# Kernel tuning notes

Hardware: AMD Instinct MI355X
Metric: run time of the kernel (lower is better)

## Reference

```python
import jax, jax.numpy as jnp
import numpy as np

HEAD_DIM = 128
INFTY_APPROX = 1e+30
ROTARY_BASE = 10000.0

B, T, M = 2, 2048, 1024
H = M // HEAD_DIM  # 8


def setup_inputs() -> dict:
    key = jax.random.key(0)
    ks = jax.random.split(key, 5)
    x = jax.random.normal(ks[0], (B, T, M), dtype=jnp.float32)
    # mu-param inits: wq zeros in the original; use small random here for a
    # non-degenerate numerical baseline, scaled like kv_init = d_model**-0.5
    scale = M ** (-0.5)
    wq = jax.random.normal(ks[1], (M, H, HEAD_DIM), dtype=jnp.float32) * scale
    wk = jax.random.normal(ks[2], (M, H, HEAD_DIM), dtype=jnp.float32) * scale
    wv = jax.random.normal(ks[3], (M, H, HEAD_DIM), dtype=jnp.float32) * scale
    wo = jax.random.normal(ks[4], (H, HEAD_DIM, M), dtype=jnp.float32) * scale
    return {"x": x, "wq": wq, "wk": wk, "wv": wv, "wo": wo}


def _rotary(x, base=ROTARY_BASE):
    # x: [..., T, W]; non-interpretable RoPE over even/odd halves of W
    length, width = x.shape[-2], x.shape[-1]
    half = width // 2
    positions = jnp.arange(length)[:, None].astype(x.dtype)          # [T,1]
    ang_freqs = jnp.power(base, -jnp.arange(half) / half)[None, :]   # [1,half]
    radians = positions * ang_freqs                                  # [T,half]
    cos = jnp.cos(radians).astype(x.dtype)
    sin = jnp.sin(radians).astype(x.dtype)
    even, odd = jnp.split(x, 2, axis=-1)
    return jnp.concatenate([even * cos - odd * sin,
                            even * sin + odd * cos], axis=-1)


def _fractional_rotary(x):
    # rotary on first half of head dim, passthrough on the rest
    rot, skip = jnp.split(x, 2, axis=-1)
    return jnp.concatenate([_rotary(rot), skip], axis=-1)


def reference(x, wq, wk, wv, wo):
    q = jnp.einsum('bim,mhd->bhid', x, wq)
    k = jnp.einsum('bim,mhd->bhid', x, wk)
    v = jnp.einsum('bim,mhd->bhid', x, wv)
    q = _fractional_rotary(q)
    k = _fractional_rotary(k)
    # mu-param attention: scale by 1/HEAD_DIM (not 1/sqrt(D))
    s = jnp.einsum('bhid,bhjd->bhij', q, k) / HEAD_DIM
    i = jnp.arange(T)[:, None]
    j = jnp.arange(T)[None, :]
    mask = (i < j).astype(s.dtype)  # strictly-upper-triangular
    s = s - jnp.asarray(INFTY_APPROX, dtype=s.dtype) * mask
    p = jax.nn.softmax(s, axis=-1)
    o = jnp.einsum('bhij,bhjd->bhid', p, v)
    r = jnp.einsum('bhid,hdm->bim', o, wo)
    return r
```

## Files before the change

kernel.cpp:

```cpp
#include <hip/hip_runtime.h>

#define T_SEQ 2048
#define MDL   1024
#define NH    8
#define HD    128
#define SPLIT 4

typedef __bf16 bf16;
typedef __bf16 bf16x8 __attribute__((ext_vector_type(8)));
typedef __bf16 bf16x4 __attribute__((ext_vector_type(4)));
typedef float  f32x4  __attribute__((ext_vector_type(4)));

#define GLB(p) ((const __attribute__((address_space(1))) void*)(p))
#define LDS(p) ((__attribute__((address_space(3))) void*)(p))

#if __has_builtin(__builtin_amdgcn_exp2f)
#define EXP2(x) __builtin_amdgcn_exp2f(x)
#else
#define EXP2(x) __expf((x) * 0.6931471805599453f)
#endif

#define QSCALE 0.011271055f


__global__ __launch_bounds__(256) void prep_kernel(
    const float* __restrict__ x,
    const float* __restrict__ wq, const float* __restrict__ wk,
    const float* __restrict__ wv, const float* __restrict__ wo,
    bf16* __restrict__ xb, bf16* __restrict__ Wt, bf16* __restrict__ Wot)
{
    __shared__ bf16 t_lds[64 * 72];
    const int tid = threadIdx.x;
    if (blockIdx.x < 2048) {
        size_t i = ((size_t)blockIdx.x * 256 + tid) * 8;
        float4 v0 = *(const float4*)(x + i);
        float4 v1 = *(const float4*)(x + i + 4);
        bf16x8 o;
        o[0]=(bf16)v0.x; o[1]=(bf16)v0.y; o[2]=(bf16)v0.z; o[3]=(bf16)v0.w;
        o[4]=(bf16)v1.x; o[5]=(bf16)v1.y; o[6]=(bf16)v1.z; o[7]=(bf16)v1.w;
        *(bf16x8*)(xb + i) = o;
        return;
    }
    const int bx = blockIdx.x - 2048;
    const int sec = bx >> 8;
    const int tile = bx & 255;
    const int k0 = (tile >> 4) * 64, n0 = (tile & 15) * 64;
    const float* src = sec == 0 ? wq : sec == 1 ? wk : sec == 2 ? wv : wo;
    bf16* dst = sec < 3 ? (Wt + (size_t)sec * MDL * MDL) : Wot;

    const int ir = tid >> 2, jc = (tid & 3) * 16;
    const float* sp = src + (size_t)(k0 + ir) * MDL + n0 + jc;
    #pragma unroll
    for (int c = 0; c < 4; ++c) {
        float4 v = *(const float4*)(sp + c * 4);
        bf16x4 o; o[0]=(bf16)v.x; o[1]=(bf16)v.y; o[2]=(bf16)v.z; o[3]=(bf16)v.w;
        *(bf16x4*)&t_lds[ir * 72 + jc + c * 4] = o;
    }
    __syncthreads();
    bf16x8 o0, o1;
    #pragma unroll
    for (int jj = 0; jj < 8; ++jj) {
        o0[jj] = t_lds[(jc + jj) * 72 + ir];
        o1[jj] = t_lds[(jc + 8 + jj) * 72 + ir];
    }
    bf16* dp = dst + (size_t)(n0 + ir) * MDL + k0 + jc;
    *(bf16x8*)dp = o0;
    *(bf16x8*)(dp + 8) = o1;
}

__global__ __launch_bounds__(256) void qkv_rope_kernel(
    const bf16* __restrict__ xb, const bf16* __restrict__ Wt,
    bf16* __restrict__ Qb, bf16* __restrict__ Kt, bf16* __restrict__ Vt)
{
    __shared__ bf16 smem[16384];
    bf16* a_lds = smem;
    bf16* b_lds = smem + 8192;

    const int tid = threadIdx.x, bx = blockIdx.x;
    const int nt = bx % 24, mt = bx / 24;
    const int n0 = nt * 128, m0 = mt * 128;
    const int section = n0 >> 10;
    const int h = (n0 & 1023) >> 7;

    const int lane = tid & 63, w = tid >> 6;
    const int quad = lane >> 4, l15 = lane & 15;
    const int wr = w >> 1, wc = w & 1;
    const int srow = lane >> 3;

    const int csw = ((lane & 7) ^ srow) * 8;
    const bf16* gA = xb + (size_t)m0 * MDL + csw;
    const bf16* gB = Wt + (size_t)n0 * MDL + csw;

    f32x4 acc[4][4] = {};

    for (int k0 = 0; k0 < MDL; k0 += 64) {
        #pragma unroll
        for (int i = 0; i < 4; ++i) {
            const int ch = w * 4 + i;
            const int row = ch * 8 + srow;
            __builtin_amdgcn_global_load_lds(GLB(gA + (size_t)row * MDL + k0),
                                             LDS(&a_lds[ch * 512]), 16, 0, 0);
            __builtin_amdgcn_global_load_lds(GLB(gB + (size_t)row * MDL + k0),
                                             LDS(&b_lds[ch * 512]), 16, 0, 0);
        }
        __syncthreads();

        #pragma unroll
        for (int hh = 0; hh < 2; ++hh) {
            bf16x8 af[4], bfr[4];
            #pragma unroll
            for (int mi = 0; mi < 4; ++mi) {
                const int ra = wr * 64 + mi * 16 + l15;
                af[mi] = *(const bf16x8*)&a_lds[ra * 64 + ((hh * 4 + quad) ^ (ra & 7)) * 8];
            }
            #pragma unroll
            for (int ni = 0; ni < 4; ++ni) {
                const int rb = wc * 64 + ni * 16 + l15;
                bfr[ni] = *(const bf16x8*)&b_lds[rb * 64 + ((hh * 4 + quad) ^ (rb & 7)) * 8];
            }
            #pragma unroll
            for (int mi = 0; mi < 4; ++mi)
                #pragma unroll
                for (int ni = 0; ni < 4; ++ni)
                    acc[mi][ni] = __builtin_amdgcn_mfma_f32_16x16x32_bf16(af[mi], bfr[ni], acc[mi][ni], 0, 0, 0);
        }
        __syncthreads();
    }

    const int bdx = m0 >> 11;
    const int t0 = m0 & (T_SEQ - 1);
    const int bh = bdx * NH + h;

    if (section == 2) {
        #pragma unroll
        for (int c = 0; c < 2; ++c) {
            if (wc == c) {
                #pragma unroll
                for (int mi = 0; mi < 4; ++mi)
                    #pragma unroll
                    for (int r = 0; r < 4; ++r) {
                        int p = 16 * quad + 4 * r + mi;
                        int base = (wr * 8 + (p >> 3)) * 512 + (p & 7);
                        #pragma unroll
                        for (int ni = 0; ni < 4; ++ni)
                            smem[base + (ni * 16 + l15) * 8] = (bf16)acc[mi][ni][r];
                    }
            }
            __syncthreads();
            {
                const int t8 = tid >> 4;
                bf16* vp = Vt + ((size_t)(bh * 32 + (t0 >> 6) + (t8 >> 3))) * 8192
                              + (t8 & 7) * 1024 + c * 512 + (tid & 15) * 32;
                #pragma unroll
                for (int k = 0; k < 4; ++k)
                    *(bf16x8*)(vp + k * 8) = *(const bf16x8*)&smem[tid * 32 + k * 8];
            }
            __syncthreads();
        }
        return;
    }

    float fr_n[2];
    #pragma unroll
    for (int ni = 0; ni < 2; ++ni)
        fr_n[ni] = __expf(-(float)(ni * 16 + l15) * 0.28782313662425573f);

    if (section == 0) {
        #pragma unroll
        for (int mi = 0; mi < 4; ++mi) {
            #pragma unroll
            for (int r = 0; r < 4; ++r) {
                int t = t0 + wr * 64 + mi * 16 + quad * 4 + r;
                bf16* orow = Qb + ((size_t)bh * T_SEQ + t) * HD;
                if (wc == 0) {
                    #pragma unroll
                    for (int ni = 0; ni < 2; ++ni) {
                        int d = ni * 16 + l15;
                        float ang = (float)t * fr_n[ni];
                        float sn = __sinf(ang), cs = __cosf(ang);
                        float ev = acc[mi][ni][r];
                        float ov = acc[mi][ni + 2][r];
                        orow[d]      = (bf16)((ev * cs - ov * sn) * QSCALE);
                        orow[d + 32] = (bf16)((ev * sn + ov * cs) * QSCALE);
                    }
                } else {
                    #pragma unroll
                    for (int ni = 0; ni < 4; ++ni)
                        orow[64 + ni * 16 + l15] = (bf16)(acc[mi][ni][r] * QSCALE);
                }
            }
        }
    } else {
        #pragma unroll
        for (int c = 0; c < 2; ++c) {
            if (wr == c) {
                #pragma unroll
                for (int mi = 0; mi < 4; ++mi) {
                    #pragma unroll
                    for (int r = 0; r < 4; ++r) {
                        int tl = mi * 16 + quad * 4 + r;
                        int t = t0 + c * 64 + tl;
                        if (wc == 0) {
                            #pragma unroll
                            for (int ni = 0; ni < 2; ++ni) {
                                int d = ni * 16 + l15;
                                float ang = (float)t * fr_n[ni];
                                float sn = __sinf(ang), cs = __cosf(ang);
                                float ev = acc[mi][ni][r];
                                float ov = acc[mi][ni + 2][r];
                                smem[(d >> 3) * 512 + tl * 8 + (d & 7)] = (bf16)(ev * cs - ov * sn);
                                int d2 = d + 32;
                                smem[(d2 >> 3) * 512 + tl * 8 + (d2 & 7)] = (bf16)(ev * sn + ov * cs);
                            }
                        } else {
                            #pragma unroll
                            for (int ni = 0; ni < 4; ++ni) {
                                int d = 64 + ni * 16 + l15;
                                smem[(d >> 3) * 512 + tl * 8 + (d & 7)] = (bf16)acc[mi][ni][r];
                            }
                        }
                    }
                }
            }
            __syncthreads();
            {
                bf16* kp = Kt + ((size_t)(bh * 32 + (t0 >> 6) + c)) * 8192 + tid * 32;
                #pragma unroll
                for (int k = 0; k < 4; ++k)
                    *(bf16x8*)(kp + k * 8) = *(const bf16x8*)&smem[tid * 32 + k * 8];
            }
            __syncthreads();
        }
    }
}

__global__ __launch_bounds__(256) void attn_kernel(
    const bf16* __restrict__ Qb, const bf16* __restrict__ Kt,
    const bf16* __restrict__ Vt, bf16* __restrict__ PO, float* __restrict__ Pl)
{
    __shared__ bf16 k_lds[8192];
    __shared__ bf16 v_lds[8192];
    __shared__ bf16 p_lds[4][32 * 72];

    const int tid = threadIdx.x, lane = tid & 63, w = tid >> 6;
    const int quad = lane >> 4, l15 = lane & 15;
    const int bx = blockIdx.x;
    const int xcd  = bx & 7;
    const int slot = bx >> 3;
    const int bh   = xcd * 2 + (slot >> 5);
    const int s0   = slot & (SPLIT - 1);
    const int ip   = (slot >> 2) & 7;
    const int tA = 2 * ip + 2;

    const bf16* Kbh = Kt + (size_t)bh * 32 * 8192;
    const bf16* Vbh = Vt + (size_t)bh * 32 * 8192;

    bf16x8 kreg[4], vreg[4];
    bf16x8 qf[2][4];
    f32x4 Of[2][8];
    float l_r[2][4];

    auto fetch = [&](int g) {
        const int jt = (g < tA) ? g : g - tA;
        const bf16* kt = Kbh + (size_t)jt * 8192 + tid * 8;
        const bf16* vt = Vbh + (size_t)jt * 8192 + tid * 8;
        #pragma unroll
        for (int k = 0; k < 4; ++k) {
            kreg[k] = *(const bf16x8*)(kt + k * 2048);
            vreg[k] = *(const bf16x8*)(vt + k * 2048);
        }
    };

    fetch(s0);
    int pqt = -1;

    #pragma unroll 1
    for (int g = s0; g < 34; g += SPLIT) {
        const int ph = (g >= tA);
        const int qt = ph ? 15 - ip : ip;
        const int jt = ph ? g - tA : g;

        if (qt != pqt) {
            if (pqt >= 0) {
                const size_t slotq = ((size_t)bh * 16 + pqt) * SPLIT + s0;
                #pragma unroll
                for (int mi = 0; mi < 2; ++mi)
                    #pragma unroll
                    for (int r = 0; r < 4; ++r) {
                        float ls = l_r[mi][r];
                        ls += __shfl_xor(ls, 1); ls += __shfl_xor(ls, 2);
                        ls += __shfl_xor(ls, 4); ls += __shfl_xor(ls, 8);
                        const int row = w * 32 + mi * 16 + quad * 4 + r;
                        if (l15 == 0) Pl[slotq * 128 + row] = ls;
                        bf16* pr = PO + (slotq * 128 + row) * 128;
                        #pragma unroll
                        for (int di = 0; di < 8; ++di)
                            pr[di * 16 + l15] = (bf16)Of[mi][di][r];
                    }
            }
            #pragma unroll
            for (int mi = 0; mi < 2; ++mi) {
                const bf16* qrow = Qb + ((size_t)bh * T_SEQ + qt * 128 + w * 32 + mi * 16 + l15) * HD + quad * 8;
                #pragma unroll
                for (int kk = 0; kk < 4; ++kk)
                    qf[mi][kk] = *(const bf16x8*)(qrow + kk * 32);
                #pragma unroll
                for (int di = 0; di < 8; ++di) Of[mi][di] = (f32x4){0.f, 0.f, 0.f, 0.f};
                #pragma unroll
                for (int r = 0; r < 4; ++r) l_r[mi][r] = 0.f;
            }
            pqt = qt;
        }

        __syncthreads();
        #pragma unroll
        for (int k = 0; k < 4; ++k) {
            *(bf16x8*)&k_lds[k * 2048 + tid * 8] = kreg[k];
            *(bf16x8*)&v_lds[k * 2048 + tid * 8] = vreg[k];
        }
        if (g + SPLIT < 34) fetch(g + SPLIT);
        __syncthreads();

        f32x4 sa[2][4] = {};
        #pragma unroll
        for (int kk = 0; kk < 4; ++kk) {
            bf16x8 kb[4];
            #pragma unroll
            for (int ni = 0; ni < 4; ++ni)
                kb[ni] = *(const bf16x8*)&k_lds[(kk * 4 + quad) * 512 + (ni * 16 + l15) * 8];
            #pragma unroll
            for (int ni = 0; ni < 4; ++ni)
                #pragma unroll
                for (int mi = 0; mi < 2; ++mi)
                    sa[mi][ni] = __builtin_amdgcn_mfma_f32_16x16x32_bf16(qf[mi][kk], kb[ni], sa[mi][ni], 0, 0, 0);
        }

        const bool diag = (jt >= 2 * qt);
        #pragma unroll
        for (int mi = 0; mi < 2; ++mi) {
            const int rowb = w * 32 + mi * 16 + quad * 4;
            #pragma unroll
            for (int r = 0; r < 4; ++r) {
                float ps = 0.f;
                bf16x4 pq;
                #pragma unroll
                for (int ni = 0; ni < 4; ++ni) {
                    float pv = EXP2(sa[mi][ni][r]);
                    if (diag && (jt * 64 + ni * 16 + l15) > (qt * 128 + rowb + r)) pv = 0.f;
                    ps += pv;
                    pq[ni] = (bf16)pv;
                }
                *(bf16x4*)&p_lds[w][(mi * 16 + quad * 4 + r) * 72 + l15 * 4] = pq;
                l_r[mi][r] += ps;
            }
        }

        #pragma unroll
        for (int kk = 0; kk < 2; ++kk) {
            bf16x8 pa[2];
            #pragma unroll
            for (int mi = 0; mi < 2; ++mi)
                pa[mi] = *(const bf16x8*)&p_lds[w][(mi * 16 + l15) * 72 + kk * 32 + quad * 8];
            #pragma unroll
            for (int di = 0; di < 8; ++di) {
                bf16x8 vb = *(const bf16x8*)&v_lds[(kk * 4 + quad) * 1024 + (di * 16 + l15) * 8];
                #pragma unroll
                for (int mi = 0; mi < 2; ++mi)
                    Of[mi][di] = __builtin_amdgcn_mfma_f32_16x16x32_bf16(pa[mi], vb, Of[mi][di], 0, 0, 0);
            }
        }
    }

    {
        const size_t slotq = ((size_t)bh * 16 + pqt) * SPLIT + s0;
        #pragma unroll
        for (int mi = 0; mi < 2; ++mi)
            #pragma unroll
            for (int r = 0; r < 4; ++r) {
                float ls = l_r[mi][r];
                ls += __shfl_xor(ls, 1); ls += __shfl_xor(ls, 2);
                ls += __shfl_xor(ls, 4); ls += __shfl_xor(ls, 8);
                const int row = w * 32 + mi * 16 + quad * 4 + r;
                if (l15 == 0) Pl[slotq * 128 + row] = ls;
                bf16* pr = PO + (slotq * 128 + row) * 128;
                #pragma unroll
                for (int di = 0; di < 8; ++di)
                    pr[di * 16 + l15] = (bf16)Of[mi][di][r];
            }
    }
}

__global__ __launch_bounds__(256) void attn_combine_kernel(
    const bf16* __restrict__ PO, const float* __restrict__ Pl,
    bf16* __restrict__ Ob)
{
    const int idx = blockIdx.x * 256 + threadIdx.x;
    const int dcol = (idx & 15) * 8;
    const int rowg = idx >> 4;
    const int bh = rowg >> 11, qrow = rowg & 2047;
    const int qt = qrow >> 7, row = qrow & 127;
    const int ns = (2 * qt + 2 < SPLIT) ? (2 * qt + 2) : SPLIT;

    float acc[8] = {};
    float l = 0.f;
    for (int s = 0; s < ns; ++s) {
        const size_t base = (((size_t)bh * 16 + qt) * SPLIT + s) * 128 + row;
        bf16x8 po = *(const bf16x8*)&PO[base * 128 + dcol];
        #pragma unroll
        for (int jj = 0; jj < 8; ++jj) acc[jj] += (float)po[jj];
        l += Pl[base];
    }
    const float inv = 1.f / l;
    const int b = bh >> 3, hh = bh & 7, t = qt * 128 + row;
    bf16x8 o;
    #pragma unroll
    for (int jj = 0; jj < 8; ++jj) o[jj] = (bf16)(acc[jj] * inv);
    *(bf16x8*)(Ob + ((size_t)(b * T_SEQ + t) * NH + hh) * HD + dcol) = o;
}

__global__ __launch_bounds__(256) void out_proj_kernel(
    const bf16* __restrict__ Ob, const bf16* __restrict__ Wot,
    float* __restrict__ out)
{
    __shared__ bf16 a_lds[128 * 64];
    __shared__ bf16 b_lds[64 * 64];

    const int tid = threadIdx.x, bx = blockIdx.x;
    const int nt = bx & 15, mt = bx >> 4;
    const int n0 = nt * 64, m0 = mt * 128;

    const int lane = tid & 63, w = tid >> 6;
    const int quad = lane >> 4, l15 = lane & 15;
    const int wr = w >> 1, wc = w & 1;
    const int srow = lane >> 3;

    const int csw = ((lane & 7) ^ srow) * 8;
    const bf16* gA = Ob  + (size_t)m0 * MDL + csw;
    const bf16* gB = Wot + (size_t)n0 * MDL + csw;

    f32x4 acc[4][2] = {};

    for (int k0 = 0; k0 < MDL; k0 += 64) {
        #pragma unroll
        for (int i = 0; i < 4; ++i) {
            const int ch = w * 4 + i;
            const int row = ch * 8 + srow;
            __builtin_amdgcn_global_load_lds(GLB(gA + (size_t)row * MDL + k0),
                                             LDS(&a_lds[ch * 512]), 16, 0, 0);
        }
        #pragma unroll
        for (int i = 0; i < 2; ++i) {
            const int ch = w * 2 + i;
            const int row = ch * 8 + srow;
            __builtin_amdgcn_global_load_lds(GLB(gB + (size_t)row * MDL + k0),
                                             LDS(&b_lds[ch * 512]), 16, 0, 0);
        }
        __syncthreads();

        #pragma unroll
        for (int hh = 0; hh < 2; ++hh) {
            bf16x8 af[4], bfr[2];
            #pragma unroll
            for (int mi = 0; mi < 4; ++mi) {
                const int ra = wr * 64 + mi * 16 + l15;
                af[mi] = *(const bf16x8*)&a_lds[ra * 64 + ((hh * 4 + quad) ^ (ra & 7)) * 8];
            }
            #pragma unroll
            for (int ni = 0; ni < 2; ++ni) {
                const int rb = wc * 32 + ni * 16 + l15;
                bfr[ni] = *(const bf16x8*)&b_lds[rb * 64 + ((hh * 4 + quad) ^ (rb & 7)) * 8];
            }
            #pragma unroll
            for (int mi = 0; mi < 4; ++mi)
                #pragma unroll
                for (int ni = 0; ni < 2; ++ni)
                    acc[mi][ni] = __builtin_amdgcn_mfma_f32_16x16x32_bf16(af[mi], bfr[ni], acc[mi][ni], 0, 0, 0);
        }
        __syncthreads();
    }

    #pragma unroll
    for (int mi = 0; mi < 4; ++mi)
        #pragma unroll
        for (int r = 0; r < 4; ++r) {
            int row_g = m0 + wr * 64 + mi * 16 + quad * 4 + r;
            float* crow = out + (size_t)row_g * MDL + n0;
            #pragma unroll
            for (int ni = 0; ni < 2; ++ni)
                crow[wc * 32 + ni * 16 + l15] = acc[mi][ni][r];
        }
}

extern "C" void kernel_launch(void* const* d_in, const int* in_sizes, int n_in,
                              void* d_out, int out_size, void* d_ws, size_t ws_size,
                              hipStream_t stream) {
    const float* x  = (const float*)d_in[0];
    const float* wq = (const float*)d_in[1];
    const float* wk = (const float*)d_in[2];
    const float* wv = (const float*)d_in[3];
    const float* wo = (const float*)d_in[4];
    float* out = (float*)d_out;

    const size_t NTOK = (size_t)2 * NH * T_SEQ * HD;
    bf16*  Qb  = (bf16*)d_ws;
    bf16*  Kt  = Qb + NTOK;
    bf16*  Vt  = Kt + NTOK;
    bf16*  Ob  = Vt + NTOK;
    bf16*  Wot = Ob + NTOK;
    bf16*  PO  = Wot + (size_t)MDL * MDL;
    float* Pl  = (float*)(PO + (size_t)16 * 16 * SPLIT * 128 * 128);

    bf16* xbuf = (bf16*)d_out;
    bf16* Wt   = xbuf + (size_t)4096 * MDL;

    prep_kernel<<<3072, 256, 0, stream>>>(x, wq, wk, wv, wo, xbuf, Wt, Wot);
    qkv_rope_kernel<<<768, 256, 0, stream>>>(xbuf, Wt, Qb, Kt, Vt);
    attn_kernel<<<16 * 8 * SPLIT, 256, 0, stream>>>(Qb, Kt, Vt, PO, Pl);
    attn_combine_kernel<<<2048, 256, 0, stream>>>(PO, Pl, Ob);
    out_proj_kernel<<<512, 256, 0, stream>>>(Ob, Wot, out);
}
```

Measured before the change: 193.5 us.

## Double-buffer LDS tiles in QKV and output projection GEMMs

Both projection GEMM kernels now use two LDS buffers. The next k-tile's global_load_lds is issued before the current tile's MFMA work, so global memory latency overlaps with compute, and the per-k-step synchronisation is restructured around the two buffers. The cost is doubled shared memory (64KB in the QKV kernel), which may lower occupancy. The epilogue in the QKV kernel may reuse smem and is unaffected.

New measurement: 190.8 us. About the same (-1.4%).

```diff
diff --git a/kernel.cpp b/kernel.cpp
--- a/kernel.cpp
+++ b/kernel.cpp
@@ -72,9 +72,9 @@
     const bf16* __restrict__ xb, const bf16* __restrict__ Wt,
     bf16* __restrict__ Qb, bf16* __restrict__ Kt, bf16* __restrict__ Vt)
 {
-    __shared__ bf16 smem[16384];
+    __shared__ bf16 smem[32768];
     bf16* a_lds = smem;
-    bf16* b_lds = smem + 8192;
+    bf16* b_lds = smem + 16384;
 
     const int tid = threadIdx.x, bx = blockIdx.x;
     const int nt = bx % 24, mt = bx / 24;
@@ -93,30 +93,31 @@
 
     f32x4 acc[4][4] = {};
 
-    for (int k0 = 0; k0 < MDL; k0 += 64) {
+    auto stage = [&](int k0, int buf) {
         #pragma unroll
         for (int i = 0; i < 4; ++i) {
             const int ch = w * 4 + i;
             const int row = ch * 8 + srow;
             __builtin_amdgcn_global_load_lds(GLB(gA + (size_t)row * MDL + k0),
-                                             LDS(&a_lds[ch * 512]), 16, 0, 0);
+                                             LDS(&a_lds[buf * 8192 + ch * 512]), 16, 0, 0);
             __builtin_amdgcn_global_load_lds(GLB(gB + (size_t)row * MDL + k0),
-                                             LDS(&b_lds[ch * 512]), 16, 0, 0);
-        }
-        __syncthreads();
-
+                                             LDS(&b_lds[buf * 8192 + ch * 512]), 16, 0, 0);
+        }
+    };
+
+    auto compute = [&](int buf) {
         #pragma unroll
         for (int hh = 0; hh < 2; ++hh) {
             bf16x8 af[4], bfr[4];
             #pragma unroll
             for (int mi = 0; mi < 4; ++mi) {
                 const int ra = wr * 64 + mi * 16 + l15;
-                af[mi] = *(const bf16x8*)&a_lds[ra * 64 + ((hh * 4 + quad) ^ (ra & 7)) * 8];
+                af[mi] = *(const bf16x8*)&a_lds[buf * 8192 + ra * 64 + ((hh * 4 + quad) ^ (ra & 7)) * 8];
             }
             #pragma unroll
             for (int ni = 0; ni < 4; ++ni) {
                 const int rb = wc * 64 + ni * 16 + l15;
-                bfr[ni] = *(const bf16x8*)&b_lds[rb * 64 + ((hh * 4 + quad) ^ (rb & 7)) * 8];
+                bfr[ni] = *(const bf16x8*)&b_lds[buf * 8192 + rb * 64 + ((hh * 4 + quad) ^ (rb & 7)) * 8];
             }
             #pragma unroll
             for (int mi = 0; mi < 4; ++mi)
@@ -124,6 +125,18 @@
                 for (int ni = 0; ni < 4; ++ni)
                     acc[mi][ni] = __builtin_amdgcn_mfma_f32_16x16x32_bf16(af[mi], bfr[ni], acc[mi][ni], 0, 0, 0);
         }
+    };
+
+    stage(0, 0);
+    __syncthreads();
+
+    #pragma unroll 1
+    for (int k0 = 0; k0 < MDL; k0 += 128) {
+        stage(k0 + 64, 1);
+        compute(0);
+        __syncthreads();
+        if (k0 + 128 < MDL) stage(k0 + 128, 0);
+        compute(1);
         __syncthreads();
     }
 
@@ -422,8 +435,8 @@
     const bf16* __restrict__ Ob, const bf16* __restrict__ Wot,
     float* __restrict__ out)
 {
-    __shared__ bf16 a_lds[128 * 64];
-    __shared__ bf16 b_lds[64 * 64];
+    __shared__ bf16 a_lds[2][128 * 64];
+    __shared__ bf16 b_lds[2][64 * 64];
 
     const int tid = threadIdx.x, bx = blockIdx.x;
     const int nt = bx & 15, mt = bx >> 4;
@@ -440,35 +453,36 @@
 
     f32x4 acc[4][2] = {};
 
-    for (int k0 = 0; k0 < MDL; k0 += 64) {
+    auto stage = [&](int k0, int buf) {
         #pragma unroll
         for (int i = 0; i < 4; ++i) {
             const int ch = w * 4 + i;
             const int row = ch * 8 + srow;
             __builtin_amdgcn_global_load_lds(GLB(gA + (size_t)row * MDL + k0),
-                                             LDS(&a_lds[ch * 512]), 16, 0, 0);
+                                             LDS(&a_lds[buf][ch * 512]), 16, 0, 0);
         }
         #pragma unroll
         for (int i = 0; i < 2; ++i) {
             const int ch = w * 2 + i;
             const int row = ch * 8 + srow;
             __builtin_amdgcn_global_load_lds(GLB(gB + (size_t)row * MDL + k0),
-                                             LDS(&b_lds[ch * 512]), 16, 0, 0);
-        }
-        __syncthreads();
-
+                                             LDS(&b_lds[buf][ch * 512]), 16, 0, 0);
+        }
+    };
+
+    auto compute = [&](int buf) {
         #pragma unroll
         for (int hh = 0; hh < 2; ++hh) {
             bf16x8 af[4], bfr[2];
             #pragma unroll
             for (int mi = 0; mi < 4; ++mi) {
                 const int ra = wr * 64 + mi * 16 + l15;
-                af[mi] = *(const bf16x8*)&a_lds[ra * 64 + ((hh * 4 + quad) ^ (ra & 7)) * 8];
+                af[mi] = *(const bf16x8*)&a_lds[buf][ra * 64 + ((hh * 4 + quad) ^ (ra & 7)) * 8];
             }
             #pragma unroll
             for (int ni = 0; ni < 2; ++ni) {
                 const int rb = wc * 32 + ni * 16 + l15;
-                bfr[ni] = *(const bf16x8*)&b_lds[rb * 64 + ((hh * 4 + quad) ^ (rb & 7)) * 8];
+                bfr[ni] = *(const bf16x8*)&b_lds[buf][rb * 64 + ((hh * 4 + quad) ^ (rb & 7)) * 8];
             }
             #pragma unroll
             for (int mi = 0; mi < 4; ++mi)
@@ -476,6 +490,18 @@
                 for (int ni = 0; ni < 2; ++ni)
                     acc[mi][ni] = __builtin_amdgcn_mfma_f32_16x16x32_bf16(af[mi], bfr[ni], acc[mi][ni], 0, 0, 0);
         }
+    };
+
+    stage(0, 0);
+    __syncthreads();
+
+    #pragma unroll 1
+    for (int k0 = 0; k0 < MDL; k0 += 128) {
+        stage(k0 + 64, 1);
+        compute(0);
+        __syncthreads();
+        if (k0 + 128 < MDL) stage(k0 + 128, 0);
+        compute(1);
         __syncthreads();
     }
 
```
